# Kernel tuning notes

Measured on AMD Instinct MI355X. Metric: run time of the kernel, lower is better.

Reference implementation:

```python
import jax, jax.numpy as jnp
import numpy as np

N_QUBITS = 8
N_LAYERS = 4
BATCH = 4096


def _ry(theta):
    # RY(theta) = [[cos(t/2), -sin(t/2)], [sin(t/2), cos(t/2)]]
    c = jnp.cos(theta / 2).astype(jnp.complex64)
    s = jnp.sin(theta / 2).astype(jnp.complex64)
    return jnp.stack([jnp.stack([c, -s], axis=-1),
                      jnp.stack([s, c], axis=-1)], axis=-2)  # (..., 2, 2)


def _rz(theta):
    # RZ(theta) = diag(exp(-i t/2), exp(+i t/2))
    p = jnp.exp(-0.5j * theta.astype(jnp.complex64))
    z = jnp.zeros_like(p)
    return jnp.stack([jnp.stack([p, z], axis=-1),
                      jnp.stack([z, jnp.conj(p)], axis=-1)], axis=-2)


def _apply_1q(state, U, w):
    # state: (B, 2, 2, ..., 2); apply 2x2 unitary U on wire w (axis 1+w).
    st = jnp.moveaxis(state, 1 + w, -1)
    if U.ndim == 3:  # per-sample (batched) gate, U: (B, 2, 2)
        st = jnp.einsum('bij,b...j->b...i', U, st)
    else:            # shared gate, U: (2, 2)
        st = jnp.einsum('ij,b...j->b...i', U, st)
    return jnp.moveaxis(st, -1, 1 + w)


def _apply_cnot(state, c, t):
    # flip target wire t where control wire c is |1>
    st = jnp.moveaxis(state, (1 + c, 1 + t), (-2, -1))
    st = jnp.concatenate([st[..., 0:1, :], st[..., 1:2, ::-1]], axis=-2)
    return jnp.moveaxis(st, (-2, -1), (1 + c, 1 + t))


def _circuit(x, weights):
    B = x.shape[0]
    state = jnp.zeros((B,) + (2,) * N_QUBITS, jnp.complex64)
    state = state.at[(slice(None),) + (0,) * N_QUBITS].set(1.0)  # |0...0>
    # Angle encoding: RY(x_i) on each wire, batched over samples
    for i in range(N_QUBITS):
        state = _apply_1q(state, _ry(x[:, i]), i)
    # Variational layers: CNOT ring then RY/RZ rotations
    for l in range(N_LAYERS):
        for i in range(N_QUBITS):
            state = _apply_cnot(state, i, (i + 1) % N_QUBITS)
        for i in range(N_QUBITS):
            state = _apply_1q(state, _ry(weights[l, i, 0]), i)
            state = _apply_1q(state, _rz(weights[l, i, 1]), i)
    # <Z_0> = P(q0=0) - P(q0=1)
    probs = jnp.sum(jnp.abs(state.reshape(B, 2, -1)) ** 2, axis=-1)
    return (probs[:, 0] - probs[:, 1]).astype(jnp.float32)


def setup_inputs() -> dict:
    key = jax.random.key(0)
    k1, k2 = jax.random.split(key)
    x = jax.random.uniform(k1, (BATCH, N_QUBITS), dtype=jnp.float32) * jnp.pi
    weights = jax.random.normal(k2, (N_LAYERS, N_QUBITS, 2), dtype=jnp.float32) * 0.1
    return {"x": x, "weights": weights}


def reference(x, weights):
    return _circuit(x, weights)
```

## Files before the change

kernel.cpp:

```cpp
#include <hip/hip_runtime.h>

#define NQ 8
#define NL 4
#define BATCH 4096


template <int CTRL>
__device__ __forceinline__ float dppx(float v) {
  return __int_as_float(
      __builtin_amdgcn_update_dpp(0, __float_as_int(v), CTRL, 0xF, 0xF, true));
}

__device__ __forceinline__ float swz16(float v) {
  return __int_as_float(__builtin_amdgcn_ds_swizzle(__float_as_int(v), 0x401F));
}
__device__ __forceinline__ float swz4(float v) {
  return __int_as_float(__builtin_amdgcn_ds_swizzle(__float_as_int(v), 0x101F));
}
__device__ __forceinline__ float swz18(float v) {
  return __int_as_float(__builtin_amdgcn_ds_swizzle(__float_as_int(v), 0x601F));
}
__device__ __forceinline__ float bperm(int addr, float v) {
  return __int_as_float(__builtin_amdgcn_ds_bpermute(addr, __float_as_int(v)));
}
__device__ __forceinline__ float rlane(float v, int l) {
  return __int_as_float(__builtin_amdgcn_readlane(__float_as_int(v), l));
}
__device__ __forceinline__ float sxor(float v, unsigned m) {
  return __int_as_float(__float_as_int(v) ^ m);
}

template <int W>
__device__ __forceinline__ float xl(float v) {
  if constexpr (W == 0) return swz16(v);
  else if constexpr (W == 1) return dppx<0x128>(v);
  else if constexpr (W == 2) return swz4(v);
  else if constexpr (W == 3) return dppx<0x4E>(v);
  else return dppx<0xB1>(v);
}

template <int W>
__device__ __forceinline__ void ry_gate(float re[8], float im[8],
                                        float c, float s, unsigned m) {
  if constexpr (W <= 4) {
    const float ss = sxor(s, m);
#pragma unroll
    for (int r = 0; r < 8; ++r) {
      float pr = xl<W>(re[r]);
      float pi = xl<W>(im[r]);
      re[r] = c * re[r] + ss * pr;
      im[r] = c * im[r] + ss * pi;
    }
  } else {
    constexpr int mm = 1 << (7 - W);
#pragma unroll
    for (int r = 0; r < 8; ++r) {
      if ((r & mm) == 0) {
        const int r1 = r | mm;
        float a0r = re[r], a1r = re[r1];
        float a0i = im[r], a1i = im[r1];
        re[r]  = c * a0r - s * a1r;
        re[r1] = s * a0r + c * a1r;
        im[r]  = c * a0i - s * a1i;
        im[r1] = s * a0i + c * a1i;
      }
    }
  }
}

template <int W>
__device__ __forceinline__ void rz_gate(float re[8], float im[8],
                                        float c, float s, unsigned m) {
  if constexpr (W <= 4) {
    const float ss = sxor(s, m);
#pragma unroll
    for (int r = 0; r < 8; ++r) {
      float nr = re[r] * c - im[r] * ss;
      float ni = im[r] * c + re[r] * ss;
      re[r] = nr; im[r] = ni;
    }
  } else {
    constexpr int mm = 1 << (7 - W);
#pragma unroll
    for (int r = 0; r < 8; ++r) {
      const float ss = (r & mm) ? s : -s;
      float nr = re[r] * c - im[r] * ss;
      float ni = im[r] * c + re[r] * ss;
      re[r] = nr; im[r] = ni;
    }
  }
}

__device__ __forceinline__ void ring2(float re[8], float im[8],
                                      int addr_e, int addr_o, bool P) {
  const float t0r = P ? re[4] : re[0], t0i = P ? im[4] : im[0];
  const float t1r = P ? re[5] : re[1], t1i = P ? im[5] : im[1];
  const float t2r = P ? re[7] : re[3], t2i = P ? im[7] : im[3];
  const float t3r = P ? re[6] : re[2], t3i = P ? im[6] : im[2];
  const float t4r = P ? re[2] : re[6], t4i = P ? im[2] : im[6];
  const float t5r = P ? re[3] : re[7], t5i = P ? im[3] : im[7];
  const float t6r = P ? re[1] : re[5], t6i = P ? im[1] : im[5];
  const float t7r = P ? re[0] : re[4], t7i = P ? im[0] : im[4];
  re[0] = bperm(addr_e, t0r); re[1] = bperm(addr_o, t1r);
  re[2] = bperm(addr_e, t2r); re[3] = bperm(addr_o, t3r);
  re[4] = bperm(addr_e, t4r); re[5] = bperm(addr_o, t5r);
  re[6] = bperm(addr_e, t6r); re[7] = bperm(addr_o, t7r);
  im[0] = bperm(addr_e, t0i); im[1] = bperm(addr_o, t1i);
  im[2] = bperm(addr_e, t2i); im[3] = bperm(addr_o, t3i);
  im[4] = bperm(addr_e, t4i); im[5] = bperm(addr_o, t5i);
  im[6] = bperm(addr_e, t6i); im[7] = bperm(addr_o, t7i);
}

__global__ __launch_bounds__(256, 2) void vqc_kernel(const float* __restrict__ x,
                                                     const float* __restrict__ w,
                                                     float* __restrict__ out) {
  const int lane = (int)(threadIdx.x & 63);
  const int wv = (int)((blockIdx.x * blockDim.x + threadIdx.x) >> 6);
  const int hl = lane & 31;

  const int ghl    = hl ^ (hl >> 1);
  const int addr_e = ((lane & 32) | ghl) << 2;
  const int addr_o = addr_e ^ 0x60;
  const bool Ppar  = (__popc(hl) & 1) != 0;

  unsigned sm[8];
#pragma unroll
  for (int W = 0; W < 5; ++W)
    sm[W] = ((lane >> (4 - W)) & 1) ? 0u : 0x80000000u;
  sm[5] = 0u; sm[6] = 0u; sm[7] = 0u;

  float sn, cs;
  {
    const float wvv = w[lane];
    const float xv  = x[(wv << 4) | (lane & 15)];
    const float ang = (lane >= 48) ? xv : wvv;
    __sincosf(ang * 0.5f, &sn, &cs);
  }
  float cy48, sy48;
  __sincosf(w[48] * 0.5f, &sy48, &cy48);

  float fc[8], fs[8];
  {
    const int fbase = (48 + ((lane >> 5) << 3)) << 2;
#pragma unroll
    for (int k = 0; k < 8; ++k) {
      fc[k] = bperm(fbase + (k << 2), cs);
      fs[k] = bperm(fbase + (k << 2), sn);
    }
  }

  float re[8], im[8];
  {
    const int HL4 = (lane >> 4) & 1, G3 = (ghl >> 3) & 1, HL0 = lane & 1;
    const float Pl = ((ghl & 4) ? fs[2] : fc[2]) *
                     ((ghl & 2) ? fs[3] : fc[3]) *
                     ((ghl & 1) ? fs[4] : fc[4]);
    const float q0 = (HL4 ? fs[0] : fc[0]) * (G3 ? fs[1] : fc[1]);
    const float q1 = (HL4 ? fc[0] : fs[0]) * (G3 ? fc[1] : fs[1]);
    const float g50 = HL0 ? fs[5] : fc[5];
    const float g51 = HL0 ? fc[5] : fs[5];
    const float a0 = Pl * q0 * g50, a1 = Pl * q1 * g50;
    const float b0 = Pl * q0 * g51, b1 = Pl * q1 * g51;
    const float cc = fc[6] * fc[7], csx = fc[6] * fs[7];
    const float sc = fs[6] * fc[7], ssx = fs[6] * fs[7];
    re[0] = a0 * cc;  re[1] = a1 * csx; re[2] = a0 * ssx; re[3] = a1 * sc;
    re[4] = b0 * sc;  re[5] = b1 * ssx; re[6] = b0 * csx; re[7] = b1 * cc;
#pragma unroll
    for (int r = 0; r < 8; ++r) im[r] = 0.f;
  }

#define APPLY_ROT(BASE, W) {                                 \
    const float cy = rlane(cs, (BASE) + (W) * 2);            \
    const float sy = rlane(sn, (BASE) + (W) * 2);            \
    const float cz = rlane(cs, (BASE) + (W) * 2 + 1);        \
    const float sz = rlane(sn, (BASE) + (W) * 2 + 1);        \
    ry_gate<W>(re, im, cy, sy, sm[W]);                       \
    rz_gate<W>(re, im, cz, sz, sm[W]); }

  {
    const float cy = rlane(cs, 0), sy = rlane(sn, 0);
    const float cz = rlane(cs, 1), sz = rlane(sn, 1);
    const float ssy = sxor(sy, sm[0]);
#pragma unroll
    for (int r = 0; r < 8; ++r) {
      float p = swz16(re[r]);
      re[r] = cy * re[r] + ssy * p;
    }
    const float ssz = sxor(sz, sm[0]);
#pragma unroll
    for (int r = 0; r < 8; ++r) {
      im[r] = ssz * re[r];
      re[r] = cz * re[r];
    }
    APPLY_ROT(0, 1) APPLY_ROT(0, 2) APPLY_ROT(0, 3)
    APPLY_ROT(0, 4) APPLY_ROT(0, 5) APPLY_ROT(0, 6) APPLY_ROT(0, 7)
  }

#pragma unroll
  for (int l = 1; l < NL - 1; ++l) {
    ring2(re, im, addr_e, addr_o, Ppar);
    const int base = l * 16;
    APPLY_ROT(base, 0) APPLY_ROT(base, 1) APPLY_ROT(base, 2) APPLY_ROT(base, 3)
    APPLY_ROT(base, 4) APPLY_ROT(base, 5) APPLY_ROT(base, 6) APPLY_ROT(base, 7)
  }
#undef APPLY_ROT

  {
    const unsigned pm0 = (unsigned)(__popc(lane & 15) & 1) << 31;
    float acc = 0.f;
#pragma unroll
    for (int r = 0; r < 8; ++r) {
      const unsigned podd =
          ((r == 1) | (r == 2) | (r == 4) | (r == 7)) ? 0x80000000u : 0u;
      const unsigned pmr = pm0 ^ podd;
      const float ssy = sxor(sy48, pmr ^ 0x80000000u);
      const float pr = swz18(re[r]);
      const float pi = swz18(im[r]);
      const float nr = cy48 * re[r] + ssy * pr;
      const float ni = cy48 * im[r] + ssy * pi;
      acc += sxor(nr * nr + ni * ni, pmr);
    }
    acc += dppx<0xB1>(acc);
    acc += dppx<0x4E>(acc);
    acc += swz4(acc);
    acc += dppx<0x128>(acc);
    acc += swz16(acc);
    if ((lane & 31) == 0) out[(wv << 1) | (lane >> 5)] = acc;
  }
}

extern "C" void kernel_launch(void* const* d_in, const int* in_sizes, int n_in,
                              void* d_out, int out_size, void* d_ws, size_t ws_size,
                              hipStream_t stream) {
  const float* x = (const float*)d_in[0];
  const float* w = (const float*)d_in[1];
  float* out = (float*)d_out;
  (void)in_sizes; (void)n_in; (void)out_size; (void)d_ws; (void)ws_size;

  dim3 grid(BATCH / 2 * 64 / 256), block(256);
  hipLaunchKernelGGL(vqc_kernel, grid, block, 0, stream, x, w, out);
}
```

Before: 61.61 us.

## Commute RZ gates past RY and merge each layer's RZs into one diagonal phase

RZ gates on different wires commute with RY gates on other wires, so all RY gates in a layer are applied first and the eight RZ gates are then combined into a single per-amplitude diagonal phase. The lane-side phase is built by summing signed half-angles and calling one sincos, and the register-side phase comes from products of cos and sin terms. In the first layer the state stays real through the RY gates, so those gates run only on the real part. This removes seven separate complex multiply passes per layer and half the RY work in layer 0, at the cost of an extra sincos and some setup arithmetic, with a small change in rounding from the merged phase.

```diff
diff --git a/kernel.cpp b/kernel.cpp
--- a/kernel.cpp
+++ b/kernel.cpp
@@ -69,24 +69,72 @@
 }
 
 template <int W>
-__device__ __forceinline__ void rz_gate(float re[8], float im[8],
-                                        float c, float s, unsigned m) {
+__device__ __forceinline__ void ry_real(float re[8], float c, float s,
+                                        unsigned m) {
   if constexpr (W <= 4) {
     const float ss = sxor(s, m);
 #pragma unroll
     for (int r = 0; r < 8; ++r) {
-      float nr = re[r] * c - im[r] * ss;
-      float ni = im[r] * c + re[r] * ss;
-      re[r] = nr; im[r] = ni;
+      float pr = xl<W>(re[r]);
+      re[r] = c * re[r] + ss * pr;
     }
   } else {
     constexpr int mm = 1 << (7 - W);
 #pragma unroll
     for (int r = 0; r < 8; ++r) {
-      const float ss = (r & mm) ? s : -s;
-      float nr = re[r] * c - im[r] * ss;
-      float ni = im[r] * c + re[r] * ss;
-      re[r] = nr; im[r] = ni;
+      if ((r & mm) == 0) {
+        const int r1 = r | mm;
+        float a0 = re[r], a1 = re[r1];
+        re[r]  = c * a0 - s * a1;
+        re[r1] = s * a0 + c * a1;
+      }
+    }
+  }
+}
+
+template <bool REAL>
+__device__ __forceinline__ void rz_diag(float re[8], float im[8],
+                                        float cs, float sn, float ha,
+                                        const unsigned* sm, int base) {
+  float phL = sxor(rlane(ha, base + 1), sm[0]);
+  phL += sxor(rlane(ha, base + 3), sm[1]);
+  phL += sxor(rlane(ha, base + 5), sm[2]);
+  phL += sxor(rlane(ha, base + 7), sm[3]);
+  phL += sxor(rlane(ha, base + 9), sm[4]);
+  float sL, cL;
+  __sincosf(phL, &sL, &cL);
+  const float c5 = rlane(cs, base + 11), s5 = rlane(sn, base + 11);
+  const float c6 = rlane(cs, base + 13), s6 = rlane(sn, base + 13);
+  const float c7 = rlane(cs, base + 15), s7 = rlane(sn, base + 15);
+  const float m1 = c5 * c6, m2 = s5 * s6, m3 = s5 * c6, m4 = c5 * s6;
+  const float ppr = m1 - m2, ppi = m3 + m4;
+  const float pmr = m1 + m2, pmi = m3 - m4;
+  float cR[4], sR[4];
+  {
+    const float a = pmr * c7, b = pmi * s7, c2 = pmi * c7, d = pmr * s7;
+    cR[0] = a + b; sR[0] = c2 - d;
+    cR[1] = a - b; sR[1] = c2 + d;
+  }
+  {
+    const float a = ppr * c7, b = ppi * s7, c2 = ppi * c7, d = ppr * s7;
+    cR[2] = a + b; sR[2] = c2 - d;
+    cR[3] = a - b; sR[3] = c2 + d;
+  }
+#pragma unroll
+  for (int r = 0; r < 8; ++r) {
+    const int k = (r < 4) ? (3 - r) : (r - 4);
+    const float cRr = cR[k];
+    const float sRr = (r < 4) ? -sR[k] : sR[k];
+    const float C = cL * cRr - sL * sRr;
+    const float S = sL * cRr + cL * sRr;
+    if constexpr (REAL) {
+      const float t = re[r];
+      re[r] = C * t;
+      im[r] = S * t;
+    } else {
+      const float tr = re[r], ti = im[r];
+      re[r] = C * tr - S * ti;
+      im[r] = C * ti + S * tr;
     }
   }
 }
@@ -123,18 +171,17 @@
   const int addr_o = addr_e ^ 0x60;
   const bool Ppar  = (__popc(hl) & 1) != 0;
 
-  unsigned sm[8];
+  unsigned sm[5];
 #pragma unroll
   for (int W = 0; W < 5; ++W)
     sm[W] = ((lane >> (4 - W)) & 1) ? 0u : 0x80000000u;
-  sm[5] = 0u; sm[6] = 0u; sm[7] = 0u;
-
-  float sn, cs;
+
+  float sn, cs, ha;
   {
     const float wvv = w[lane];
     const float xv  = x[(wv << 4) | (lane & 15)];
-    const float ang = (lane >= 48) ? xv : wvv;
-    __sincosf(ang * 0.5f, &sn, &cs);
+    ha = ((lane >= 48) ? xv : wvv) * 0.5f;
+    __sincosf(ha, &sn, &cs);
   }
   float cy48, sy48;
   __sincosf(w[48] * 0.5f, &sy48, &cy48);
@@ -165,45 +212,32 @@
     const float sc = fs[6] * fc[7], ssx = fs[6] * fs[7];
     re[0] = a0 * cc;  re[1] = a1 * csx; re[2] = a0 * ssx; re[3] = a1 * sc;
     re[4] = b0 * sc;  re[5] = b1 * ssx; re[6] = b0 * csx; re[7] = b1 * cc;
-#pragma unroll
-    for (int r = 0; r < 8; ++r) im[r] = 0.f;
-  }
-
-#define APPLY_ROT(BASE, W) {                                 \
-    const float cy = rlane(cs, (BASE) + (W) * 2);            \
-    const float sy = rlane(sn, (BASE) + (W) * 2);            \
-    const float cz = rlane(cs, (BASE) + (W) * 2 + 1);        \
-    const float sz = rlane(sn, (BASE) + (W) * 2 + 1);        \
-    ry_gate<W>(re, im, cy, sy, sm[W]);                       \
-    rz_gate<W>(re, im, cz, sz, sm[W]); }
-
-  {
-    const float cy = rlane(cs, 0), sy = rlane(sn, 0);
-    const float cz = rlane(cs, 1), sz = rlane(sn, 1);
-    const float ssy = sxor(sy, sm[0]);
-#pragma unroll
-    for (int r = 0; r < 8; ++r) {
-      float p = swz16(re[r]);
-      re[r] = cy * re[r] + ssy * p;
-    }
-    const float ssz = sxor(sz, sm[0]);
-#pragma unroll
-    for (int r = 0; r < 8; ++r) {
-      im[r] = ssz * re[r];
-      re[r] = cz * re[r];
-    }
-    APPLY_ROT(0, 1) APPLY_ROT(0, 2) APPLY_ROT(0, 3)
-    APPLY_ROT(0, 4) APPLY_ROT(0, 5) APPLY_ROT(0, 6) APPLY_ROT(0, 7)
-  }
+  }
+
+  ry_real<0>(re, rlane(cs, 0),  rlane(sn, 0),  sm[0]);
+  ry_real<1>(re, rlane(cs, 2),  rlane(sn, 2),  sm[1]);
+  ry_real<2>(re, rlane(cs, 4),  rlane(sn, 4),  sm[2]);
+  ry_real<3>(re, rlane(cs, 6),  rlane(sn, 6),  sm[3]);
+  ry_real<4>(re, rlane(cs, 8),  rlane(sn, 8),  sm[4]);
+  ry_real<5>(re, rlane(cs, 10), rlane(sn, 10), 0u);
+  ry_real<6>(re, rlane(cs, 12), rlane(sn, 12), 0u);
+  ry_real<7>(re, rlane(cs, 14), rlane(sn, 14), 0u);
+  rz_diag<true>(re, im, cs, sn, ha, sm, 0);
 
 #pragma unroll
   for (int l = 1; l < NL - 1; ++l) {
     ring2(re, im, addr_e, addr_o, Ppar);
     const int base = l * 16;
-    APPLY_ROT(base, 0) APPLY_ROT(base, 1) APPLY_ROT(base, 2) APPLY_ROT(base, 3)
-    APPLY_ROT(base, 4) APPLY_ROT(base, 5) APPLY_ROT(base, 6) APPLY_ROT(base, 7)
-  }
-#undef APPLY_ROT
+    ry_gate<0>(re, im, rlane(cs, base + 0),  rlane(sn, base + 0),  sm[0]);
+    ry_gate<1>(re, im, rlane(cs, base + 2),  rlane(sn, base + 2),  sm[1]);
+    ry_gate<2>(re, im, rlane(cs, base + 4),  rlane(sn, base + 4),  sm[2]);
+    ry_gate<3>(re, im, rlane(cs, base + 6),  rlane(sn, base + 6),  sm[3]);
+    ry_gate<4>(re, im, rlane(cs, base + 8),  rlane(sn, base + 8),  sm[4]);
+    ry_gate<5>(re, im, rlane(cs, base + 10), rlane(sn, base + 10), 0u);
+    ry_gate<6>(re, im, rlane(cs, base + 12), rlane(sn, base + 12), 0u);
+    ry_gate<7>(re, im, rlane(cs, base + 14), rlane(sn, base + 14), 0u);
+    rz_diag<false>(re, im, cs, sn, ha, sm, base);
+  }
 
   {
     const unsigned pm0 = (unsigned)(__popc(lane & 15) & 1) << 31;
```

New measurement: 60.11 us. -2.4%, faster.
